# Kernel optimization log

Hardware: AMD Instinct MI355X
Metric: run time of the kernel (lower is better)

Reference implementation:

```python
import jax, jax.numpy as jnp
import numpy as np

B, T, D = 2, 4096, 512
H = 8  # heads; head_dim = D // H = 64


def setup_inputs() -> dict:
    key = jax.random.key(0)
    ks = jax.random.split(key, 8)
    s = 0.02
    return {
        "queries": jax.random.normal(ks[0], (B, T, D), jnp.float32),
        "keys": jax.random.normal(ks[1], (B, T, D), jnp.float32),
        "values": jax.random.normal(ks[2], (B, T, D), jnp.float32),
        "Wq": jax.random.normal(ks[3], (D, D), jnp.float32) * s,
        "Wk": jax.random.normal(ks[4], (D, D), jnp.float32) * s,
        "Wv": jax.random.normal(ks[5], (D, D), jnp.float32) * s,
        "Wo": jax.random.normal(ks[6], (D, D), jnp.float32) * s,
        "bo": jnp.zeros((D,), jnp.float32),
    }


def reference(queries, keys, values, Wq, Wk, Wv, Wo, bo):
    # pad_dim = 0 for in_dim=512, n_heads=8, so no padding needed.
    Bq, Tq, _ = queries.shape
    Ts = keys.shape[1]
    hd = D // H
    # torch Linear: x @ W.T
    q = (queries @ Wq.T).reshape(Bq, Tq, H, hd).transpose(0, 2, 1, 3)  # [B,H,T,hd]
    k = (keys @ Wk.T).reshape(Bq, Ts, H, hd).transpose(0, 2, 1, 3)
    v = (values @ Wv.T).reshape(Bq, Ts, H, hd).transpose(0, 2, 1, 3)
    attn = jnp.einsum("bhtd,bhsd->bhts", q, k) / np.sqrt(hd).astype(np.float32)
    attn = jax.nn.softmax(attn, axis=-1)  # [B,H,T,Ts]
    z = jnp.einsum("bhts,bhsd->bhtd", attn, v)
    z = z.transpose(0, 2, 1, 3).reshape(Bq, Tq, D)
    out = z @ Wo.T + bo
    return (out, attn)
```

## Files before the change

kernel.cpp:

```cpp
#include <hip/hip_runtime.h>

typedef __attribute__((ext_vector_type(8))) short bf16x8;
typedef __attribute__((ext_vector_type(8))) unsigned short u16x8;
typedef __attribute__((ext_vector_type(4))) float f32x4;

#define DEVINL __device__ __forceinline__

constexpr int TB = 2;
constexpr int TT = 4096;
constexpr int TD = 512;
constexpr int TH = 8;
constexpr int THD = 64;
constexpr int TM = TB * TT;

DEVINL unsigned short f2b(float f) {
  unsigned u = __builtin_bit_cast(unsigned, f);
  u += 0x7FFFu + ((u >> 16) & 1u);
  return (unsigned short)(u >> 16);
}

template<int FINAL>
__global__ __launch_bounds__(256, 2)
void gemm_xwt(const float* __restrict__ X, const float* __restrict__ W,
              unsigned short* __restrict__ Yb, float* __restrict__ Yf,
              const float* __restrict__ bias)
{
  constexpr int K = TD, N = TD;
  __shared__ unsigned short As[128][72];
  __shared__ unsigned short Bs[128][72];

  const int t    = threadIdx.x;
  const int lane = t & 63, w = t >> 6;
  const int fr = lane & 15, fq = lane >> 4;
  const int wr = (w >> 1) * 64, wc = (w & 1) * 64;
  const int bm = blockIdx.x * 128, bn = blockIdx.y * 128;
  const int srow = t >> 1;
  const int skh  = (t & 1) * 32;

  f32x4 acc[4][4];
  #pragma unroll
  for (int m = 0; m < 4; ++m)
    #pragma unroll
    for (int n = 0; n < 4; ++n)
      acc[m][n] = f32x4{0.f, 0.f, 0.f, 0.f};

  for (int k0 = 0; k0 < K; k0 += 64) {
    const float* srcA = X + (size_t)(bm + srow) * K + k0 + skh;
    const float* srcB = W + (size_t)(bn + srow) * K + k0 + skh;
    #pragma unroll
    for (int i = 0; i < 4; ++i) {
      float4 a0 = ((const float4*)srcA)[2 * i];
      float4 a1 = ((const float4*)srcA)[2 * i + 1];
      u16x8 oa = {f2b(a0.x), f2b(a0.y), f2b(a0.z), f2b(a0.w),
                  f2b(a1.x), f2b(a1.y), f2b(a1.z), f2b(a1.w)};
      *(u16x8*)&As[srow][skh + i * 8] = oa;
      float4 b0 = ((const float4*)srcB)[2 * i];
      float4 b1 = ((const float4*)srcB)[2 * i + 1];
      u16x8 ob = {f2b(b0.x), f2b(b0.y), f2b(b0.z), f2b(b0.w),
                  f2b(b1.x), f2b(b1.y), f2b(b1.z), f2b(b1.w)};
      *(u16x8*)&Bs[srow][skh + i * 8] = ob;
    }
    __syncthreads();
    #pragma unroll
    for (int kk = 0; kk < 2; ++kk) {
      bf16x8 af[4], bfv[4];
      #pragma unroll
      for (int m = 0; m < 4; ++m)
        af[m] = *(const bf16x8*)&As[wr + m * 16 + fr][kk * 32 + fq * 8];
      #pragma unroll
      for (int n = 0; n < 4; ++n)
        bfv[n] = *(const bf16x8*)&Bs[wc + n * 16 + fr][kk * 32 + fq * 8];
      #pragma unroll
      for (int m = 0; m < 4; ++m)
        #pragma unroll
        for (int n = 0; n < 4; ++n)
          acc[m][n] = __builtin_amdgcn_mfma_f32_16x16x32_bf16(af[m], bfv[n], acc[m][n], 0, 0, 0);
    }
    __syncthreads();
  }

  #pragma unroll
  for (int m = 0; m < 4; ++m) {
    const int gm = bm + wr + m * 16 + fq * 4;
    #pragma unroll
    for (int n = 0; n < 4; ++n) {
      const int gn = bn + wc + n * 16 + fr;
      #pragma unroll
      for (int i = 0; i < 4; ++i) {
        float v = acc[m][n][i];
        if (FINAL) Yf[(size_t)(gm + i) * N + gn] = v + bias[gn];
        else       Yb[(size_t)(gm + i) * N + gn] = f2b(v);
      }
    }
  }
}

__global__ __launch_bounds__(256, 2)
void attn_fused(const unsigned short* __restrict__ Qb,
                const unsigned short* __restrict__ Kb,
                const unsigned short* __restrict__ Vb,
                float* __restrict__ attnO, float* __restrict__ Z)
{
  __shared__ unsigned short Qs[64][72];
  __shared__ unsigned short Ks[2][64][72];
  __shared__ unsigned short VTs[2][64][72];
  __shared__ unsigned short Ps[4][16][72];

  const int t    = threadIdx.x;
  const int lane = t & 63, w = t >> 6;
  const int fr = lane & 15, fq = lane >> 4;
  const int bh = blockIdx.y;
  const int b  = bh >> 3, h = bh & 7;
  const int q0 = blockIdx.x * 64;

  const size_t rowQ  = ((size_t)(b * TT + q0)) * TD + h * THD;
  const size_t rowKV = ((size_t)(b * TT)) * TD + h * THD;

  const int tr = t >> 2;
  const int tc = (t & 3) * 16;

  auto loadT = [&](const unsigned short* base, int kv0, u16x8& r0, u16x8& r1) {
    const unsigned short* src = base + rowKV + (size_t)(kv0 + tr) * TD + tc;
    r0 = *(const u16x8*)src;
    r1 = *(const u16x8*)(src + 8);
  };
  auto writeK = [&](int buf, const u16x8& r0, const u16x8& r1) {
    *(u16x8*)&Ks[buf][tr][tc]     = r0;
    *(u16x8*)&Ks[buf][tr][tc + 8] = r1;
  };
  auto writeVT = [&](int buf, const u16x8& r0, const u16x8& r1) {
    #pragma unroll
    for (int i = 0; i < 8; ++i) VTs[buf][tc + i][tr] = r0[i];
    #pragma unroll
    for (int i = 0; i < 8; ++i) VTs[buf][tc + 8 + i][tr] = r1[i];
  };

  {
    const unsigned short* src = Qb + rowQ + (size_t)tr * TD + tc;
    *(u16x8*)&Qs[tr][tc]     = *(const u16x8*)src;
    *(u16x8*)&Qs[tr][tc + 8] = *(const u16x8*)(src + 8);
  }
  u16x8 kr0, kr1, vr0, vr1;
  loadT(Kb, 0, kr0, kr1);
  writeK(0, kr0, kr1);
  __syncthreads();

  bf16x8 aq[2];
  aq[0] = *(const bf16x8*)&Qs[w * 16 + fr][fq * 8];
  aq[1] = *(const bf16x8*)&Qs[w * 16 + fr][32 + fq * 8];

  constexpr int NT = TT / 64;
  constexpr float SC = 0.125f;

  float lsum[4] = {0.f, 0.f, 0.f, 0.f};
  for (int j = 0; j < NT; ++j) {
    const int cur = j & 1;
    if (j + 1 < NT) loadT(Kb, (j + 1) * 64, kr0, kr1);
    #pragma unroll
    for (int n = 0; n < 4; ++n) {
      f32x4 s = f32x4{0.f, 0.f, 0.f, 0.f};
      #pragma unroll
      for (int kk = 0; kk < 2; ++kk) {
        bf16x8 bk = *(const bf16x8*)&Ks[cur][n * 16 + fr][kk * 32 + fq * 8];
        s = __builtin_amdgcn_mfma_f32_16x16x32_bf16(aq[kk], bk, s, 0, 0, 0);
      }
      #pragma unroll
      for (int i = 0; i < 4; ++i) lsum[i] += __expf(s[i] * SC);
    }
    if (j + 1 < NT) writeK(cur ^ 1, kr0, kr1);
    __syncthreads();
  }
  #pragma unroll
  for (int msk = 1; msk <= 8; msk <<= 1)
    #pragma unroll
    for (int i = 0; i < 4; ++i) lsum[i] += __shfl_xor(lsum[i], msk, 64);
  float rinv[4];
  #pragma unroll
  for (int i = 0; i < 4; ++i) rinv[i] = 1.0f / lsum[i];

  loadT(Kb, 0, kr0, kr1);
  loadT(Vb, 0, vr0, vr1);
  writeK(0, kr0, kr1);
  writeVT(0, vr0, vr1);
  __syncthreads();

  f32x4 accz[4];
  #pragma unroll
  for (int n = 0; n < 4; ++n) accz[n] = f32x4{0.f, 0.f, 0.f, 0.f};

  const size_t abase = ((size_t)bh * TT + q0 + w * 16 + fq * 4) * TT + fr;

  for (int j = 0; j < NT; ++j) {
    const int cur = j & 1;
    const int kv0 = j * 64;
    if (j + 1 < NT) {
      loadT(Kb, (j + 1) * 64, kr0, kr1);
      loadT(Vb, (j + 1) * 64, vr0, vr1);
    }
    #pragma unroll
    for (int n = 0; n < 4; ++n) {
      f32x4 s = f32x4{0.f, 0.f, 0.f, 0.f};
      #pragma unroll
      for (int kk = 0; kk < 2; ++kk) {
        bf16x8 bk = *(const bf16x8*)&Ks[cur][n * 16 + fr][kk * 32 + fq * 8];
        s = __builtin_amdgcn_mfma_f32_16x16x32_bf16(aq[kk], bk, s, 0, 0, 0);
      }
      #pragma unroll
      for (int i = 0; i < 4; ++i) {
        float p = __expf(s[i] * SC) * rinv[i];
        attnO[abase + (size_t)i * TT + kv0 + n * 16] = p;
        Ps[w][fq * 4 + i][n * 16 + fr] = f2b(p);
      }
    }
    asm volatile("s_waitcnt lgkmcnt(0)" ::: "memory");
    __builtin_amdgcn_sched_barrier(0);
    #pragma unroll
    for (int kk = 0; kk < 2; ++kk) {
      bf16x8 ap = *(const bf16x8*)&Ps[w][fr][kk * 32 + fq * 8];
      #pragma unroll
      for (int n = 0; n < 4; ++n) {
        bf16x8 bv = *(const bf16x8*)&VTs[cur][n * 16 + fr][kk * 32 + fq * 8];
        accz[n] = __builtin_amdgcn_mfma_f32_16x16x32_bf16(ap, bv, accz[n], 0, 0, 0);
      }
    }
    if (j + 1 < NT) {
      writeK(cur ^ 1, kr0, kr1);
      writeVT(cur ^ 1, vr0, vr1);
    }
    __syncthreads();
  }

  const size_t zbase = ((size_t)(b * TT + q0 + w * 16 + fq * 4)) * TD + h * THD + fr;
  #pragma unroll
  for (int n = 0; n < 4; ++n)
    #pragma unroll
    for (int i = 0; i < 4; ++i)
      Z[zbase + (size_t)i * TD + n * 16] = accz[n][i];
}

extern "C" void kernel_launch(void* const* d_in, const int* in_sizes, int n_in,
                              void* d_out, int out_size, void* d_ws, size_t ws_size,
                              hipStream_t stream) {
  const float* queries = (const float*)d_in[0];
  const float* keys    = (const float*)d_in[1];
  const float* values  = (const float*)d_in[2];
  const float* Wq = (const float*)d_in[3];
  const float* Wk = (const float*)d_in[4];
  const float* Wv = (const float*)d_in[5];
  const float* Wo = (const float*)d_in[6];
  const float* bo = (const float*)d_in[7];

  float* out  = (float*)d_out;
  float* attn = out + (size_t)TM * TD;

  unsigned short* qb = (unsigned short*)d_ws;
  unsigned short* kb = qb + (size_t)TM * TD;
  unsigned short* vb = kb + (size_t)TM * TD;
  float*          zf = (float*)(vb + (size_t)TM * TD);

  dim3 gg(TM / 128, TD / 128), bb(256);
  gemm_xwt<0><<<gg, bb, 0, stream>>>(queries, Wq, qb, nullptr, nullptr);
  gemm_xwt<0><<<gg, bb, 0, stream>>>(keys,    Wk, kb, nullptr, nullptr);
  gemm_xwt<0><<<gg, bb, 0, stream>>>(values,  Wv, vb, nullptr, nullptr);

  attn_fused<<<dim3(TT / 64, TB * TH), bb, 0, stream>>>(qb, kb, vb, attn, zf);

  gemm_xwt<1><<<gg, bb, 0, stream>>>(zf, Wo, nullptr, out, bo);
}
```

Measured before the change: 594.1 us.

## Emit V projection pre-transposed per head and use lighter barriers in attention

```diff
diff --git a/kernel.cpp b/kernel.cpp
--- a/kernel.cpp
+++ b/kernel.cpp
@@ -19,7 +19,13 @@
   return (unsigned short)(u >> 16);
 }
 
-template<int FINAL>
+DEVINL void lgkm_barrier() {
+  asm volatile("s_waitcnt lgkmcnt(0)" ::: "memory");
+  __builtin_amdgcn_s_barrier();
+  __builtin_amdgcn_sched_barrier(0);
+}
+
+template<int MODE>
 __global__ __launch_bounds__(256, 2)
 void gemm_xwt(const float* __restrict__ X, const float* __restrict__ W,
               unsigned short* __restrict__ Yb, float* __restrict__ Yf,
@@ -39,10 +45,10 @@
 
   f32x4 acc[4][4];
   #pragma unroll
-  for (int m = 0; m < 4; ++m)
-    #pragma unroll
-    for (int n = 0; n < 4; ++n)
-      acc[m][n] = f32x4{0.f, 0.f, 0.f, 0.f};
+  for (int i = 0; i < 4; ++i)
+    #pragma unroll
+    for (int j = 0; j < 4; ++j)
+      acc[i][j] = f32x4{0.f, 0.f, 0.f, 0.f};
 
   for (int k0 = 0; k0 < K; k0 += 64) {
     const float* srcA = X + (size_t)(bm + srow) * K + k0 + skh;
@@ -65,31 +71,43 @@
     for (int kk = 0; kk < 2; ++kk) {
       bf16x8 af[4], bfv[4];
       #pragma unroll
-      for (int m = 0; m < 4; ++m)
-        af[m] = *(const bf16x8*)&As[wr + m * 16 + fr][kk * 32 + fq * 8];
-      #pragma unroll
-      for (int n = 0; n < 4; ++n)
-        bfv[n] = *(const bf16x8*)&Bs[wc + n * 16 + fr][kk * 32 + fq * 8];
-      #pragma unroll
-      for (int m = 0; m < 4; ++m)
+      for (int i = 0; i < 4; ++i)
+        af[i] = *(const bf16x8*)&As[wr + i * 16 + fr][kk * 32 + fq * 8];
+      #pragma unroll
+      for (int j = 0; j < 4; ++j)
+        bfv[j] = *(const bf16x8*)&Bs[wc + j * 16 + fr][kk * 32 + fq * 8];
+      #pragma unroll
+      for (int i = 0; i < 4; ++i)
         #pragma unroll
-        for (int n = 0; n < 4; ++n)
-          acc[m][n] = __builtin_amdgcn_mfma_f32_16x16x32_bf16(af[m], bfv[n], acc[m][n], 0, 0, 0);
+        for (int j = 0; j < 4; ++j) {
+          if (MODE == 2)
+            acc[i][j] = __builtin_amdgcn_mfma_f32_16x16x32_bf16(bfv[i], af[j], acc[i][j], 0, 0, 0);
+          else
+            acc[i][j] = __builtin_amdgcn_mfma_f32_16x16x32_bf16(af[i], bfv[j], acc[i][j], 0, 0, 0);
+        }
     }
     __syncthreads();
   }
 
   #pragma unroll
-  for (int m = 0; m < 4; ++m) {
-    const int gm = bm + wr + m * 16 + fq * 4;
-    #pragma unroll
-    for (int n = 0; n < 4; ++n) {
-      const int gn = bn + wc + n * 16 + fr;
-      #pragma unroll
-      for (int i = 0; i < 4; ++i) {
-        float v = acc[m][n][i];
-        if (FINAL) Yf[(size_t)(gm + i) * N + gn] = v + bias[gn];
-        else       Yb[(size_t)(gm + i) * N + gn] = f2b(v);
+  for (int i = 0; i < 4; ++i) {
+    #pragma unroll
+    for (int j = 0; j < 4; ++j) {
+      #pragma unroll
+      for (int ii = 0; ii < 4; ++ii) {
+        float v = acc[i][j][ii];
+        if (MODE == 2) {
+          const int Nidx = bn + wc + i * 16 + fq * 4 + ii;
+          const int Midx = bm + wr + j * 16 + fr;
+          const int h = Nidx >> 6, d = Nidx & (THD - 1);
+          const int b = Midx >> 12, tt = Midx & (TT - 1);
+          Yb[((size_t)(b * TH + h) * THD + d) * TT + tt] = f2b(v);
+        } else {
+          const int gm = bm + wr + i * 16 + fq * 4 + ii;
+          const int gn = bn + wc + j * 16 + fr;
+          if (MODE == 1) Yf[(size_t)gm * N + gn] = v + bias[gn];
+          else           Yb[(size_t)gm * N + gn] = f2b(v);
+        }
       }
     }
   }
@@ -98,7 +116,7 @@
 __global__ __launch_bounds__(256, 2)
 void attn_fused(const unsigned short* __restrict__ Qb,
                 const unsigned short* __restrict__ Kb,
-                const unsigned short* __restrict__ Vb,
+                const unsigned short* __restrict__ VTg,
                 float* __restrict__ attnO, float* __restrict__ Z)
 {
   __shared__ unsigned short Qs[64][72];
@@ -115,12 +133,18 @@
 
   const size_t rowQ  = ((size_t)(b * TT + q0)) * TD + h * THD;
   const size_t rowKV = ((size_t)(b * TT)) * TD + h * THD;
+  const size_t vtBase = (size_t)bh * THD * TT;
 
   const int tr = t >> 2;
   const int tc = (t & 3) * 16;
 
-  auto loadT = [&](const unsigned short* base, int kv0, u16x8& r0, u16x8& r1) {
-    const unsigned short* src = base + rowKV + (size_t)(kv0 + tr) * TD + tc;
+  auto loadK = [&](int kv0, u16x8& r0, u16x8& r1) {
+    const unsigned short* src = Kb + rowKV + (size_t)(kv0 + tr) * TD + tc;
+    r0 = *(const u16x8*)src;
+    r1 = *(const u16x8*)(src + 8);
+  };
+  auto loadVT = [&](int kv0, u16x8& r0, u16x8& r1) {
+    const unsigned short* src = VTg + vtBase + (size_t)tr * TT + kv0 + tc;
     r0 = *(const u16x8*)src;
     r1 = *(const u16x8*)(src + 8);
   };
@@ -129,10 +153,8 @@
     *(u16x8*)&Ks[buf][tr][tc + 8] = r1;
   };
   auto writeVT = [&](int buf, const u16x8& r0, const u16x8& r1) {
-    #pragma unroll
-    for (int i = 0; i < 8; ++i) VTs[buf][tc + i][tr] = r0[i];
-    #pragma unroll
-    for (int i = 0; i < 8; ++i) VTs[buf][tc + 8 + i][tr] = r1[i];
+    *(u16x8*)&VTs[buf][tr][tc]     = r0;
+    *(u16x8*)&VTs[buf][tr][tc + 8] = r1;
   };
 
   {
@@ -141,9 +163,9 @@
     *(u16x8*)&Qs[tr][tc + 8] = *(const u16x8*)(src + 8);
   }
   u16x8 kr0, kr1, vr0, vr1;
-  loadT(Kb, 0, kr0, kr1);
+  loadK(0, kr0, kr1);
   writeK(0, kr0, kr1);
-  __syncthreads();
+  lgkm_barrier();
 
   bf16x8 aq[2];
   aq[0] = *(const bf16x8*)&Qs[w * 16 + fr][fq * 8];
@@ -155,7 +177,7 @@
   float lsum[4] = {0.f, 0.f, 0.f, 0.f};
   for (int j = 0; j < NT; ++j) {
     const int cur = j & 1;
-    if (j + 1 < NT) loadT(Kb, (j + 1) * 64, kr0, kr1);
+    if (j + 1 < NT) loadK((j + 1) * 64, kr0, kr1);
     #pragma unroll
     for (int n = 0; n < 4; ++n) {
       f32x4 s = f32x4{0.f, 0.f, 0.f, 0.f};
@@ -168,7 +190,7 @@
       for (int i = 0; i < 4; ++i) lsum[i] += __expf(s[i] * SC);
     }
     if (j + 1 < NT) writeK(cur ^ 1, kr0, kr1);
-    __syncthreads();
+    lgkm_barrier();
   }
   #pragma unroll
   for (int msk = 1; msk <= 8; msk <<= 1)
@@ -178,11 +200,11 @@
   #pragma unroll
   for (int i = 0; i < 4; ++i) rinv[i] = 1.0f / lsum[i];
 
-  loadT(Kb, 0, kr0, kr1);
-  loadT(Vb, 0, vr0, vr1);
+  loadK(0, kr0, kr1);
+  loadVT(0, vr0, vr1);
   writeK(0, kr0, kr1);
   writeVT(0, vr0, vr1);
-  __syncthreads();
+  lgkm_barrier();
 
   f32x4 accz[4];
   #pragma unroll
@@ -194,8 +216,8 @@
     const int cur = j & 1;
     const int kv0 = j * 64;
     if (j + 1 < NT) {
-      loadT(Kb, (j + 1) * 64, kr0, kr1);
-      loadT(Vb, (j + 1) * 64, vr0, vr1);
+      loadK((j + 1) * 64, kr0, kr1);
+      loadVT((j + 1) * 64, vr0, vr1);
     }
     #pragma unroll
     for (int n = 0; n < 4; ++n) {
@@ -208,7 +230,7 @@
       #pragma unroll
       for (int i = 0; i < 4; ++i) {
         float p = __expf(s[i] * SC) * rinv[i];
-        attnO[abase + (size_t)i * TT + kv0 + n * 16] = p;
+        __builtin_nontemporal_store(p, &attnO[abase + (size_t)i * TT + kv0 + n * 16]);
         Ps[w][fq * 4 + i][n * 16 + fr] = f2b(p);
       }
     }
@@ -227,7 +249,7 @@
       writeK(cur ^ 1, kr0, kr1);
       writeVT(cur ^ 1, vr0, vr1);
     }
-    __syncthreads();
+    lgkm_barrier();
   }
 
   const size_t zbase = ((size_t)(b * TT + q0 + w * 16 + fq * 4)) * TD + h * THD + fr;
@@ -255,15 +277,15 @@
 
   unsigned short* qb = (unsigned short*)d_ws;
   unsigned short* kb = qb + (size_t)TM * TD;
-  unsigned short* vb = kb + (size_t)TM * TD;
-  float*          zf = (float*)(vb + (size_t)TM * TD);
+  unsigned short* vt = kb + (size_t)TM * TD;
+  float*          zf = (float*)(vt + (size_t)TM * TD);
 
   dim3 gg(TM / 128, TD / 128), bb(256);
   gemm_xwt<0><<<gg, bb, 0, stream>>>(queries, Wq, qb, nullptr, nullptr);
   gemm_xwt<0><<<gg, bb, 0, stream>>>(keys,    Wk, kb, nullptr, nullptr);
-  gemm_xwt<0><<<gg, bb, 0, stream>>>(values,  Wv, vb, nullptr, nullptr);
-
-  attn_fused<<<dim3(TT / 64, TB * TH), bb, 0, stream>>>(qb, kb, vb, attn, zf);
+  gemm_xwt<2><<<gg, bb, 0, stream>>>(values,  Wv, vt, nullptr, nullptr);
+
+  attn_fused<<<dim3(TT / 64, TB * TH), bb, 0, stream>>>(qb, kb, vt, attn, zf);
 
   gemm_xwt<1><<<gg, bb, 0, stream>>>(zf, Wo, nullptr, out, bo);
 }
```

Measured after the change: 545.4 us. 1.09x faster.
